# Performance work log

Measured on AMD Instinct MI355X. Metric: run time of the kernel, lower is better.

## Reference

```python
import jax, jax.numpy as jnp
import numpy as np

C = 128
L = 4
NEG_SLOPE = 0.2


def _head(x, rb_w, rb_b, out_w, out_b):
    # x: [T, C]; rb_w: [2, 2, C, C] (block, layer) in torch Linear (out,in) layout.
    for i in range(2):
        h = jax.nn.leaky_relu(x @ rb_w[i, 0].T + rb_b[i, 0], NEG_SLOPE)
        h = h @ rb_w[i, 1].T + rb_b[i, 1]
        x = jax.nn.leaky_relu(x + h, NEG_SLOPE)  # act(shortcut + l2(act(l1(x))))
    return x @ out_w.T + out_b


def setup_inputs() -> dict:
    key = jax.random.key(0)
    ks = iter(jax.random.split(key, 32))
    s = 0.05  # small init so the relu-RNN recurrence stays stable over 32768 steps

    def w(shape):
        return jax.random.normal(next(ks), shape, jnp.float32) * s

    inp = {
        "x": jax.random.normal(next(ks), (C,), jnp.float32),
        "W_ih": w((L, C, C)),
        "W_hh": w((L, C, C)),
        "b_ih": w((L, C)),
        "b_hh": w((L, C)),
    }
    for name, out_dim in [("atom", 8), ("pos", 1), ("mag", 1)]:
        inp[name + "_rb_w"] = w((2, 2, C, C))
        inp[name + "_rb_b"] = w((2, 2, C))
        inp[name + "_w"] = w((out_dim, C))
        inp[name + "_b"] = w((out_dim,))
    inp["max_steps"] = 32768
    return inp


def reference(x, W_ih, W_hh, b_ih, b_hh,
              atom_rb_w, atom_rb_b, atom_w, atom_b,
              pos_rb_w, pos_rb_b, pos_w, pos_b,
              mag_rb_w, mag_rb_b, mag_w, mag_b,
              max_steps):
    # hid[0] = x (conditioning), other layers start at zero; first input is zeros.
    hid0 = jnp.zeros((L, C), x.dtype).at[0].set(x)
    inp0 = jnp.zeros((C,), x.dtype)

    def step(carry, _):
        xin, hid = carry  # xin: [C], hid: [L, C]
        cur = xin
        hs = []
        for l in range(L):
            cur = jax.nn.relu(cur @ W_ih[l].T + b_ih[l] + hid[l] @ W_hh[l].T + b_hh[l])
            hs.append(cur)
        new_hid = jnp.stack(hs)
        return (cur, new_hid), cur  # top-layer output is the next step's input

    _, encodings = jax.lax.scan(step, (inp0, hid0), None, length=max_steps)  # [T, C]

    atoms = _head(encodings, atom_rb_w, atom_rb_b, atom_w, atom_b)  # [T, 8]
    pos = _head(encodings, pos_rb_w, pos_rb_b, pos_w, pos_b)        # [T, 1]
    mags = _head(encodings, mag_rb_w, mag_rb_b, mag_w, mag_b)       # [T, 1]
    return jnp.concatenate([atoms, pos, mags], axis=-1)             # [T, 10]
```

## Files before the change

kernel.cpp:

```cpp
#include <hip/hip_runtime.h>
#include <cstdint>

typedef uint32_t u32;
typedef _Float16 f16;
typedef f16 f16x2 __attribute__((ext_vector_type(2)));
typedef f16 f16x8 __attribute__((ext_vector_type(8)));
typedef float f32x4 __attribute__((ext_vector_type(4)));

static __device__ __forceinline__ u32 pack2(float a, float b) {
    f16x2 v;
    v.x = (f16)a;
    v.y = (f16)b;
    return __builtin_bit_cast(u32, v);
}

static __device__ __forceinline__ float dot2(u32 a, u32 b, float c) {
    return __builtin_amdgcn_fdot2(__builtin_bit_cast(f16x2, a),
                                  __builtin_bit_cast(f16x2, b), c, false);
}

static __device__ __forceinline__ unsigned short f16bits(float v) {
    return __builtin_bit_cast(unsigned short, (f16)v);
}

#define BAR() asm volatile("s_waitcnt lgkmcnt(0)\n\ts_barrier" ::: "memory")

#define MFMA(A, B, C) __builtin_amdgcn_mfma_f32_16x16x32_f16(A, B, C, 0, 0, 0)

__global__ __launch_bounds__(256, 1) void rnn_kernel(
    const float* __restrict__ x0,
    const float* __restrict__ Wih, const float* __restrict__ Whh,
    const float* __restrict__ bih, const float* __restrict__ bhh,
    u32* __restrict__ enc, int T)
{
    __shared__ u32 buf[2][4][64];

    const int tid  = threadIdx.x;
    const int w    = tid >> 6;
    const int lane = tid & 63;
    const int m    = lane & 15;
    const int g    = lane >> 4;

    f16x8 a[4][2][8];
    f32x4 bias[4][2];
    #pragma unroll
    for (int l = 0; l < 4; ++l) {
        #pragma unroll
        for (int t = 0; t < 2; ++t) {
            const int row = w * 32 + t * 16 + m;
            #pragma unroll
            for (int kt = 0; kt < 8; ++kt) {
                const float* W = (kt < 4) ? Wih : Whh;
                const float* p = W + ((size_t)(l * 128 + row)) * 128
                                   + (kt & 3) * 32 + g * 8;
                f16x8 v;
                #pragma unroll
                for (int e = 0; e < 8; ++e) v[e] = (f16)p[e];
                a[l][t][kt] = v;
            }
            const int r4 = w * 32 + t * 16 + g * 4;
            f32x4 b;
            #pragma unroll
            for (int r = 0; r < 4; ++r)
                b[r] = bih[l * 128 + r4 + r] + bhh[l * 128 + r4 + r];
            bias[l][t] = b;
        }
    }

    if (tid < 64)       buf[1][0][tid] = pack2(x0[2 * tid], x0[2 * tid + 1]);
    else if (tid < 256) ((u32*)buf[1])[tid] = 0u;
    __syncthreads();

    f16x8 hpA[4], hpB[4];
    {
        const u32* h0 = &buf[1][0][0];
        #pragma unroll
        for (int j = 0; j < 4; ++j)
            hpA[j] = *(const f16x8*)(h0 + j * 16 + g * 4);
    }

#define SLOT(l, HIN, HOUT, CURB, NXTB, STORE_ENC) do {                        \
        const u32* _cb = (CURB);                                              \
        const u32* _nb = (NXTB);                                              \
        f16x8 i0 = *(const f16x8*)(_cb + 0 * 16 + g * 4);                     \
        f16x8 i1 = *(const f16x8*)(_cb + 1 * 16 + g * 4);                     \
        f16x8 i2 = *(const f16x8*)(_cb + 2 * 16 + g * 4);                     \
        f16x8 i3 = *(const f16x8*)(_cb + 3 * 16 + g * 4);                     \
        HOUT[0] = *(const f16x8*)(_nb + 0 * 16 + g * 4);                      \
        HOUT[1] = *(const f16x8*)(_nb + 1 * 16 + g * 4);                      \
        HOUT[2] = *(const f16x8*)(_nb + 2 * 16 + g * 4);                      \
        HOUT[3] = *(const f16x8*)(_nb + 3 * 16 + g * 4);                      \
        u32* _wb = &buf[_p][l][0];                                            \
        _Pragma("unroll")                                                     \
        for (int t = 0; t < 2; ++t) {                                         \
            f32x4 c0 = bias[l][t];                                            \
            f32x4 c1 = {0.f, 0.f, 0.f, 0.f};                                  \
            c0 = MFMA(a[l][t][4], HIN[0], c0);            \
            c1 = MFMA(a[l][t][5], HIN[1], c1);                                \
            c0 = MFMA(a[l][t][6], HIN[2], c0);                                \
            c1 = MFMA(a[l][t][7], HIN[3], c1);                                \
            c0 = MFMA(a[l][t][0], i0, c0);              \
            c1 = MFMA(a[l][t][1], i1, c1);                                    \
            c0 = MFMA(a[l][t][2], i2, c0);                                    \
            c1 = MFMA(a[l][t][3], i3, c1);                                    \
            f32x4 d = c0 + c1;                                                \
            float y0 = fmaxf(d[0], 0.f), y1 = fmaxf(d[1], 0.f);               \
            float y2 = fmaxf(d[2], 0.f), y3 = fmaxf(d[3], 0.f);               \
            u32 w0 = pack2(y0, y1), w1 = pack2(y2, y3);                       \
            if (m == 0) {                                                     \
                *(uint2*)(_wb + w * 16 + t * 8 + g * 2) = make_uint2(w0, w1); \
                if (STORE_ENC)                                                \
                    *(uint2*)(enc + (size_t)s * 64 + w * 16 + t * 8 + g * 2)  \
                        = make_uint2(w0, w1);                                 \
            }                                                                 \
        }                                                                     \
        BAR();                                                                \
    } while (0)

    for (int s = 0; s < T; ++s) {
        const int _p = s & 1;
        const int _q = _p ^ 1;
        SLOT(0, hpA, hpB, &buf[_q][3][0], &buf[_q][1][0], 0);
        SLOT(1, hpB, hpA, &buf[_p][0][0], &buf[_q][2][0], 0);
        SLOT(2, hpA, hpB, &buf[_p][1][0], &buf[_q][3][0], 0);
        SLOT(3, hpB, hpA, &buf[_p][2][0], &buf[_p][0][0], 1);
    }
#undef SLOT
}

__global__ __launch_bounds__(256) void heads_kernel(
    const u32* __restrict__ enc,
    const float* __restrict__ arw, const float* __restrict__ arb,
    const float* __restrict__ aw,  const float* __restrict__ ab,
    const float* __restrict__ prw, const float* __restrict__ prb,
    const float* __restrict__ pw,  const float* __restrict__ pb,
    const float* __restrict__ mrw, const float* __restrict__ mrb,
    const float* __restrict__ mw,  const float* __restrict__ mb,
    float* __restrict__ out, int T)
{
    const int head = blockIdx.x;
    const int r0 = blockIdx.y * 32;
    if (r0 >= T) return;

    const float *rbw, *rbb, *ow, *ob;
    int od, oc;
    if (head == 0)      { rbw = arw; rbb = arb; ow = aw; ob = ab; od = 8; oc = 0; }
    else if (head == 1) { rbw = prw; rbb = prb; ow = pw; ob = pb; od = 1; oc = 8; }
    else                { rbw = mrw; rbb = mrb; ow = mw; ob = mb; od = 1; oc = 9; }

    __shared__ u32 xs[32][64];
    __shared__ u32 hs[32][64];

    const int tid = threadIdx.x;

    #pragma unroll
    for (int rep = 0; rep < 8; ++rep) {
        int u = tid + rep * 256;
        int row = u >> 6, p = u & 63;
        xs[row][p] = enc[(size_t)(r0 + row) * 64 + p];
    }
    __syncthreads();

    const int j = tid & 127;
    const int rh = tid >> 7;

    float acc[16];
    u32 wreg[64];

#define PACKW(WPTR) do {                                                    \
        const float* _w = (WPTR);                                           \
        _Pragma("unroll")                                                   \
        for (int cc = 0; cc < 16; ++cc) {                                   \
            float4 aa = *(const float4*)(_w + cc * 8);                      \
            float4 bb = *(const float4*)(_w + cc * 8 + 4);                  \
            wreg[cc * 4 + 0] = pack2(aa.x, aa.y);                           \
            wreg[cc * 4 + 1] = pack2(aa.z, aa.w);                           \
            wreg[cc * 4 + 2] = pack2(bb.x, bb.y);                           \
            wreg[cc * 4 + 3] = pack2(bb.z, bb.w);                           \
        }                                                                   \
    } while (0)

#define MM16(SRC) do {                                                      \
        _Pragma("unroll")                                                   \
        for (int r = 0; r < 16; ++r) acc[r] = 0.f;                          \
        _Pragma("unroll")                                                   \
        for (int kp = 0; kp < 16; ++kp) {                                   \
            u32 w0 = wreg[kp * 4 + 0], w1 = wreg[kp * 4 + 1];               \
            u32 w2 = wreg[kp * 4 + 2], w3 = wreg[kp * 4 + 3];               \
            _Pragma("unroll")                                               \
            for (int r = 0; r < 16; ++r) {                                  \
                uint4 x4 = *(const uint4*)(&SRC[rh * 16 + r][kp * 4]);      \
                acc[r] = dot2(x4.x, w0, acc[r]);                            \
                acc[r] = dot2(x4.y, w1, acc[r]);                            \
                acc[r] = dot2(x4.z, w2, acc[r]);                            \
                acc[r] = dot2(x4.w, w3, acc[r]);                            \
            }                                                               \
        }                                                                   \
    } while (0)

    #pragma unroll
    for (int blk = 0; blk < 2; ++blk) {
        PACKW(rbw + (size_t)((blk * 2 + 0) * 128 + j) * 128);
        MM16(xs);
        {
            float b1 = rbb[(blk * 2 + 0) * 128 + j];
            #pragma unroll
            for (int r = 0; r < 16; ++r) {
                float v = acc[r] + b1;
                v = fmaxf(v, 0.2f * v);
                reinterpret_cast<unsigned short*>(&hs[rh * 16 + r][0])[j] = f16bits(v);
            }
        }
        __syncthreads();

        PACKW(rbw + (size_t)((blk * 2 + 1) * 128 + j) * 128);
        MM16(hs);
        {
            float b2 = rbb[(blk * 2 + 1) * 128 + j];
            #pragma unroll
            for (int r = 0; r < 16; ++r) {
                int row = rh * 16 + r;
                unsigned short xb =
                    reinterpret_cast<const unsigned short*>(&xs[row][0])[j];
                float xold = (float)__builtin_bit_cast(f16, xb);
                float v = xold + acc[r] + b2;
                v = fmaxf(v, 0.2f * v);
                reinterpret_cast<unsigned short*>(&xs[row][0])[j] = f16bits(v);
            }
        }
        __syncthreads();
    }

    {
        const int o = tid & 15;
        const int rr = tid >> 4;
        if (o < od) {
            PACKW(ow + (size_t)o * 128);
            float obv = ob[o];
            #pragma unroll
            for (int rs = 0; rs < 2; ++rs) {
                const int row = rr * 2 + rs;
                float a = 0.f;
                #pragma unroll
                for (int kp = 0; kp < 64; ++kp) a = dot2(xs[row][kp], wreg[kp], a);
                out[(size_t)(r0 + row) * 10 + oc + o] = a + obv;
            }
        }
    }
#undef PACKW
#undef MM16
}

extern "C" void kernel_launch(void* const* d_in, const int* in_sizes, int n_in,
                              void* d_out, int out_size, void* d_ws, size_t ws_size,
                              hipStream_t stream)
{
    const float* x   = (const float*)d_in[0];
    const float* Wih = (const float*)d_in[1];
    const float* Whh = (const float*)d_in[2];
    const float* bih = (const float*)d_in[3];
    const float* bhh = (const float*)d_in[4];
    const float* arw = (const float*)d_in[5];
    const float* arb = (const float*)d_in[6];
    const float* aw  = (const float*)d_in[7];
    const float* ab  = (const float*)d_in[8];
    const float* prw = (const float*)d_in[9];
    const float* prb = (const float*)d_in[10];
    const float* pw  = (const float*)d_in[11];
    const float* pb  = (const float*)d_in[12];
    const float* mrw = (const float*)d_in[13];
    const float* mrb = (const float*)d_in[14];
    const float* mw  = (const float*)d_in[15];
    const float* mb  = (const float*)d_in[16];

    const int T = out_size / 10;
    u32* enc = (u32*)d_ws;

    rnn_kernel<<<1, 256, 0, stream>>>(x, Wih, Whh, bih, bhh, enc, T);

    heads_kernel<<<dim3(3, (T + 31) / 32), 256, 0, stream>>>(
        enc, arw, arb, aw, ab, prw, prb, pw, pb, mrw, mrb, mw, mb,
        (float*)d_out, T);
}
```

Before: 39.85 ms.

## Precompute next layer's recurrent term with dot2 off the MFMA critical path

The hidden-to-hidden matvec for the next layer is moved out of the serial per-layer MFMA chain. It is now computed one slot ahead with packed fp16 dot2 instructions on weights held in registers and stored to shared memory as a preactivation. Each slot's critical path then shrinks to four dependent MFMAs on the input term plus the ReLU. In exchange each slot does extra VALU work, holds many more registers (128 u32 of recurrent weights per thread), and adds a shared-memory round trip and a lane shuffle.

```diff
diff --git a/kernel.cpp b/kernel.cpp
--- a/kernel.cpp
+++ b/kernel.cpp
@@ -34,98 +34,142 @@
     u32* __restrict__ enc, int T)
 {
     __shared__ u32 buf[2][4][64];
+    __shared__ float pre[4][128];
 
     const int tid  = threadIdx.x;
     const int w    = tid >> 6;
     const int lane = tid & 63;
     const int m    = lane & 15;
     const int g    = lane >> 4;
-
-    f16x8 a[4][2][8];
-    f32x4 bias[4][2];
+    const int rsh  = w * 32 + (lane >> 1);
+    const int kh   = lane & 1;
+
+    const f32x4 ZERO4 = {0.f, 0.f, 0.f, 0.f};
+
+    f16x8 ihA[4][2][4];
     #pragma unroll
-    for (int l = 0; l < 4; ++l) {
+    for (int l = 0; l < 4; ++l)
         #pragma unroll
         for (int t = 0; t < 2; ++t) {
             const int row = w * 32 + t * 16 + m;
             #pragma unroll
-            for (int kt = 0; kt < 8; ++kt) {
-                const float* W = (kt < 4) ? Wih : Whh;
-                const float* p = W + ((size_t)(l * 128 + row)) * 128
-                                   + (kt & 3) * 32 + g * 8;
+            for (int kt = 0; kt < 4; ++kt) {
+                const float* p = Wih + ((size_t)(l * 128 + row)) * 128
+                                     + kt * 32 + g * 8;
                 f16x8 v;
                 #pragma unroll
                 for (int e = 0; e < 8; ++e) v[e] = (f16)p[e];
-                a[l][t][kt] = v;
+                ihA[l][t][kt] = v;
             }
-            const int r4 = w * 32 + t * 16 + g * 4;
-            f32x4 b;
-            #pragma unroll
-            for (int r = 0; r < 4; ++r)
-                b[r] = bih[l * 128 + r4 + r] + bhh[l * 128 + r4 + r];
-            bias[l][t] = b;
         }
+
+    u32 whd[4][32];
+    float bsh[4];
+    #pragma unroll
+    for (int l = 0; l < 4; ++l) {
+        const float* p = Whh + ((size_t)(l * 128 + rsh)) * 128 + kh * 64;
+        #pragma unroll
+        for (int j = 0; j < 32; ++j)
+            whd[l][j] = pack2(p[2 * j], p[2 * j + 1]);
+        bsh[l] = bih[l * 128 + rsh] + bhh[l * 128 + rsh];
     }
 
     if (tid < 64)       buf[1][0][tid] = pack2(x0[2 * tid], x0[2 * tid + 1]);
     else if (tid < 256) ((u32*)buf[1])[tid] = 0u;
     __syncthreads();
 
-    f16x8 hpA[4], hpB[4];
+#define SHADOW(L, SRC, VOUT) do {                                             \
+        const u32* _hb = &(SRC)[kh * 32];                                     \
+        uint4 h0 = *(const uint4*)(_hb + 0);                                  \
+        uint4 h1 = *(const uint4*)(_hb + 4);                                  \
+        uint4 h2 = *(const uint4*)(_hb + 8);                                  \
+        uint4 h3 = *(const uint4*)(_hb + 12);                                 \
+        uint4 h4 = *(const uint4*)(_hb + 16);                                 \
+        uint4 h5 = *(const uint4*)(_hb + 20);                                 \
+        uint4 h6 = *(const uint4*)(_hb + 24);                                 \
+        uint4 h7 = *(const uint4*)(_hb + 28);                                 \
+        const u32* _wd = whd[L];                                              \
+        float va = kh ? 0.f : bsh[L], vb = 0.f, vc = 0.f, vd = 0.f;           \
+        va = dot2(h0.x, _wd[0], va);  vb = dot2(h0.y, _wd[1], vb);            \
+        vc = dot2(h0.z, _wd[2], vc);  vd = dot2(h0.w, _wd[3], vd);            \
+        va = dot2(h1.x, _wd[4], va);  vb = dot2(h1.y, _wd[5], vb);            \
+        vc = dot2(h1.z, _wd[6], vc);  vd = dot2(h1.w, _wd[7], vd);            \
+        va = dot2(h2.x, _wd[8], va);  vb = dot2(h2.y, _wd[9], vb);            \
+        vc = dot2(h2.z, _wd[10], vc); vd = dot2(h2.w, _wd[11], vd);           \
+        va = dot2(h3.x, _wd[12], va); vb = dot2(h3.y, _wd[13], vb);           \
+        vc = dot2(h3.z, _wd[14], vc); vd = dot2(h3.w, _wd[15], vd);           \
+        va = dot2(h4.x, _wd[16], va); vb = dot2(h4.y, _wd[17], vb);           \
+        vc = dot2(h4.z, _wd[18], vc); vd = dot2(h4.w, _wd[19], vd);           \
+        va = dot2(h5.x, _wd[20], va); vb = dot2(h5.y, _wd[21], vb);           \
+        vc = dot2(h5.z, _wd[22], vc); vd = dot2(h5.w, _wd[23], vd);           \
+        va = dot2(h6.x, _wd[24], va); vb = dot2(h6.y, _wd[25], vb);           \
+        vc = dot2(h6.z, _wd[26], vc); vd = dot2(h6.w, _wd[27], vd);           \
+        va = dot2(h7.x, _wd[28], va); vb = dot2(h7.y, _wd[29], vb);           \
+        vc = dot2(h7.z, _wd[30], vc); vd = dot2(h7.w, _wd[31], vd);           \
+        float _v = (va + vb) + (vc + vd);                                     \
+        _v += __shfl_xor(_v, 1);                                              \
+        VOUT = _v;                                                            \
+    } while (0)
+
     {
-        const u32* h0 = &buf[1][0][0];
-        #pragma unroll
-        for (int j = 0; j < 4; ++j)
-            hpA[j] = *(const f16x8*)(h0 + j * 16 + g * 4);
-    }
-
-#define SLOT(l, HIN, HOUT, CURB, NXTB, STORE_ENC) do {                        \
+        float v;
+        SHADOW(0, buf[1][0], v);
+        if (kh == 0) pre[0][rsh] = v;
+    }
+    __syncthreads();
+
+#define SLOT(l, CURB, SHSRC, STORE_ENC) do {                                  \
+        const int lnx = (l + 1) & 3;                                          \
         const u32* _cb = (CURB);                                              \
-        const u32* _nb = (NXTB);                                              \
+        f32x4 pA = *(const f32x4*)&pre[l][w * 32 + g * 4];                    \
+        f32x4 pB = *(const f32x4*)&pre[l][w * 32 + 16 + g * 4];               \
         f16x8 i0 = *(const f16x8*)(_cb + 0 * 16 + g * 4);                     \
         f16x8 i1 = *(const f16x8*)(_cb + 1 * 16 + g * 4);                     \
         f16x8 i2 = *(const f16x8*)(_cb + 2 * 16 + g * 4);                     \
         f16x8 i3 = *(const f16x8*)(_cb + 3 * 16 + g * 4);                     \
-        HOUT[0] = *(const f16x8*)(_nb + 0 * 16 + g * 4);                      \
-        HOUT[1] = *(const f16x8*)(_nb + 1 * 16 + g * 4);                      \
-        HOUT[2] = *(const f16x8*)(_nb + 2 * 16 + g * 4);                      \
-        HOUT[3] = *(const f16x8*)(_nb + 3 * 16 + g * 4);                      \
+        f32x4 cA0 = MFMA(ihA[l][0][0], i0, pA);                               \
+        f32x4 cB0 = MFMA(ihA[l][0][1], i1, ZERO4);                            \
+        f32x4 cA1 = MFMA(ihA[l][1][0], i0, pB);                               \
+        f32x4 cB1 = MFMA(ihA[l][1][1], i1, ZERO4);                            \
+        cA0 = MFMA(ihA[l][0][2], i2, cA0);                                    \
+        cB0 = MFMA(ihA[l][0][3], i3, cB0);                                    \
+        cA1 = MFMA(ihA[l][1][2], i2, cA1);                                    \
+        cB1 = MFMA(ihA[l][1][3], i3, cB1);                                    \
+        float shv;                                                            \
+        SHADOW(lnx, SHSRC, shv);               \
+        f32x4 d0 = cA0 + cB0;                                                 \
+        f32x4 d1 = cA1 + cB1;                                                 \
         u32* _wb = &buf[_p][l][0];                                            \
-        _Pragma("unroll")                                                     \
-        for (int t = 0; t < 2; ++t) {                                         \
-            f32x4 c0 = bias[l][t];                                            \
-            f32x4 c1 = {0.f, 0.f, 0.f, 0.f};                                  \
-            c0 = MFMA(a[l][t][4], HIN[0], c0);            \
-            c1 = MFMA(a[l][t][5], HIN[1], c1);                                \
-            c0 = MFMA(a[l][t][6], HIN[2], c0);                                \
-            c1 = MFMA(a[l][t][7], HIN[3], c1);                                \
-            c0 = MFMA(a[l][t][0], i0, c0);              \
-            c1 = MFMA(a[l][t][1], i1, c1);                                    \
-            c0 = MFMA(a[l][t][2], i2, c0);                                    \
-            c1 = MFMA(a[l][t][3], i3, c1);                                    \
-            f32x4 d = c0 + c1;                                                \
-            float y0 = fmaxf(d[0], 0.f), y1 = fmaxf(d[1], 0.f);               \
-            float y2 = fmaxf(d[2], 0.f), y3 = fmaxf(d[3], 0.f);               \
-            u32 w0 = pack2(y0, y1), w1 = pack2(y2, y3);                       \
+        {                                                                     \
+            u32 w0 = pack2(fmaxf(d0[0], 0.f), fmaxf(d0[1], 0.f));             \
+            u32 w1 = pack2(fmaxf(d0[2], 0.f), fmaxf(d0[3], 0.f));             \
+            u32 w2 = pack2(fmaxf(d1[0], 0.f), fmaxf(d1[1], 0.f));             \
+            u32 w3 = pack2(fmaxf(d1[2], 0.f), fmaxf(d1[3], 0.f));             \
             if (m == 0) {                                                     \
-                *(uint2*)(_wb + w * 16 + t * 8 + g * 2) = make_uint2(w0, w1); \
-                if (STORE_ENC)                                                \
-                    *(uint2*)(enc + (size_t)s * 64 + w * 16 + t * 8 + g * 2)  \
+                *(uint2*)(_wb + w * 16 + g * 2) = make_uint2(w0, w1);         \
+                *(uint2*)(_wb + w * 16 + 8 + g * 2) = make_uint2(w2, w3);     \
+                if (STORE_ENC) {                                              \
+                    *(uint2*)(enc + (size_t)s * 64 + w * 16 + g * 2)          \
                         = make_uint2(w0, w1);                                 \
+                    *(uint2*)(enc + (size_t)s * 64 + w * 16 + 8 + g * 2)      \
+                        = make_uint2(w2, w3);                                 \
+                }                                                             \
             }                                                                 \
         }                                                                     \
+        if (kh == 0) pre[lnx][rsh] = shv;                                     \
         BAR();                                                                \
     } while (0)
 
     for (int s = 0; s < T; ++s) {
         const int _p = s & 1;
         const int _q = _p ^ 1;
-        SLOT(0, hpA, hpB, &buf[_q][3][0], &buf[_q][1][0], 0);
-        SLOT(1, hpB, hpA, &buf[_p][0][0], &buf[_q][2][0], 0);
-        SLOT(2, hpA, hpB, &buf[_p][1][0], &buf[_q][3][0], 0);
-        SLOT(3, hpB, hpA, &buf[_p][2][0], &buf[_p][0][0], 1);
+        SLOT(0, &buf[_q][3][0], buf[_q][1], 0);
+        SLOT(1, &buf[_p][0][0], buf[_q][2], 0);
+        SLOT(2, &buf[_p][1][0], buf[_q][3], 0);
+        SLOT(3, &buf[_p][2][0], buf[_p][0], 1);
     }
 #undef SLOT
+#undef SHADOW
 }
 
 __global__ __launch_bounds__(256) void heads_kernel(
```

After: 54.50 ms. 1.37x slower.

## Split RNN layer into off-critical-path W_hh MFMA and dot2 W_ih chain

Applied to the files above, without the earlier changes.

Each layer's recurrent W_hh·h term is now computed with MFMA one slot ahead and parked in shared memory, so it runs off the serial dependency chain. The input term W_ih·x on the critical path is done with per-thread packed fp16 dot2 products over half-rows, combined with a lane shuffle, which is meant to cut the latency of each dependent layer step. The step loop is unrolled by two with fixed buffer parities. The cost is more register pressure (W_ih held as 128 packed words per thread) and extra shared-memory traffic for the precomputed sums.

```diff
diff --git a/kernel.cpp b/kernel.cpp
--- a/kernel.cpp
+++ b/kernel.cpp
@@ -34,96 +34,144 @@
     u32* __restrict__ enc, int T)
 {
     __shared__ u32 buf[2][4][64];
+    __shared__ float pre[4][128];
 
     const int tid  = threadIdx.x;
     const int w    = tid >> 6;
     const int lane = tid & 63;
+    const int rsh  = w * 32 + (lane >> 1);
+    const int kh   = lane & 1;
     const int m    = lane & 15;
     const int g    = lane >> 4;
 
-    f16x8 a[4][2][8];
-    f32x4 bias[4][2];
+    u32 wih[4][32];
     #pragma unroll
     for (int l = 0; l < 4; ++l) {
+        const float* p = Wih + ((size_t)(l * 128 + rsh)) * 128 + kh * 64;
+        #pragma unroll
+        for (int j = 0; j < 32; ++j)
+            wih[l][j] = pack2(p[2 * j], p[2 * j + 1]);
+    }
+
+    f16x8 hhA[4][2][4];
+    f32x4 biasT[4][2];
+    #pragma unroll
+    for (int l = 0; l < 4; ++l)
         #pragma unroll
         for (int t = 0; t < 2; ++t) {
             const int row = w * 32 + t * 16 + m;
             #pragma unroll
-            for (int kt = 0; kt < 8; ++kt) {
-                const float* W = (kt < 4) ? Wih : Whh;
-                const float* p = W + ((size_t)(l * 128 + row)) * 128
-                                   + (kt & 3) * 32 + g * 8;
+            for (int kt = 0; kt < 4; ++kt) {
+                const float* p = Whh + ((size_t)(l * 128 + row)) * 128
+                                     + kt * 32 + g * 8;
                 f16x8 v;
                 #pragma unroll
                 for (int e = 0; e < 8; ++e) v[e] = (f16)p[e];
-                a[l][t][kt] = v;
+                hhA[l][t][kt] = v;
             }
             const int r4 = w * 32 + t * 16 + g * 4;
             f32x4 b;
             #pragma unroll
             for (int r = 0; r < 4; ++r)
                 b[r] = bih[l * 128 + r4 + r] + bhh[l * 128 + r4 + r];
-            bias[l][t] = b;
-        }
-    }
+            biasT[l][t] = b;
+        }
 
     if (tid < 64)       buf[1][0][tid] = pack2(x0[2 * tid], x0[2 * tid + 1]);
     else if (tid < 256) ((u32*)buf[1])[tid] = 0u;
     __syncthreads();
 
-    f16x8 hpA[4], hpB[4];
     {
-        const u32* h0 = &buf[1][0][0];
-        #pragma unroll
-        for (int j = 0; j < 4; ++j)
-            hpA[j] = *(const f16x8*)(h0 + j * 16 + g * 4);
-    }
-
-#define SLOT(l, HIN, HOUT, CURB, NXTB, STORE_ENC) do {                        \
-        const u32* _cb = (CURB);                                              \
-        const u32* _nb = (NXTB);                                              \
-        f16x8 i0 = *(const f16x8*)(_cb + 0 * 16 + g * 4);                     \
-        f16x8 i1 = *(const f16x8*)(_cb + 1 * 16 + g * 4);                     \
-        f16x8 i2 = *(const f16x8*)(_cb + 2 * 16 + g * 4);                     \
-        f16x8 i3 = *(const f16x8*)(_cb + 3 * 16 + g * 4);                     \
-        HOUT[0] = *(const f16x8*)(_nb + 0 * 16 + g * 4);                      \
-        HOUT[1] = *(const f16x8*)(_nb + 1 * 16 + g * 4);                      \
-        HOUT[2] = *(const f16x8*)(_nb + 2 * 16 + g * 4);                      \
-        HOUT[3] = *(const f16x8*)(_nb + 3 * 16 + g * 4);                      \
-        u32* _wb = &buf[_p][l][0];                                            \
-        _Pragma("unroll")                                                     \
-        for (int t = 0; t < 2; ++t) {                                         \
-            f32x4 c0 = bias[l][t];                                            \
-            f32x4 c1 = {0.f, 0.f, 0.f, 0.f};                                  \
-            c0 = MFMA(a[l][t][4], HIN[0], c0);            \
-            c1 = MFMA(a[l][t][5], HIN[1], c1);                                \
-            c0 = MFMA(a[l][t][6], HIN[2], c0);                                \
-            c1 = MFMA(a[l][t][7], HIN[3], c1);                                \
-            c0 = MFMA(a[l][t][0], i0, c0);              \
-            c1 = MFMA(a[l][t][1], i1, c1);                                    \
-            c0 = MFMA(a[l][t][2], i2, c0);                                    \
-            c1 = MFMA(a[l][t][3], i3, c1);                                    \
-            f32x4 d = c0 + c1;                                                \
-            float y0 = fmaxf(d[0], 0.f), y1 = fmaxf(d[1], 0.f);               \
-            float y2 = fmaxf(d[2], 0.f), y3 = fmaxf(d[3], 0.f);               \
-            u32 w0 = pack2(y0, y1), w1 = pack2(y2, y3);                       \
-            if (m == 0) {                                                     \
-                *(uint2*)(_wb + w * 16 + t * 8 + g * 2) = make_uint2(w0, w1); \
-                if (STORE_ENC)                                                \
-                    *(uint2*)(enc + (size_t)s * 64 + w * 16 + t * 8 + g * 2)  \
-                        = make_uint2(w0, w1);                                 \
-            }                                                                 \
+        const u32* sb = &buf[1][0][0];
+        f16x8 j0 = *(const f16x8*)(sb + 0 * 16 + g * 4);
+        f16x8 j1 = *(const f16x8*)(sb + 1 * 16 + g * 4);
+        f16x8 j2 = *(const f16x8*)(sb + 2 * 16 + g * 4);
+        f16x8 j3 = *(const f16x8*)(sb + 3 * 16 + g * 4);
+        f32x4 t0 = MFMA(hhA[0][0][0], j0, biasT[0][0]);
+        t0 = MFMA(hhA[0][0][1], j1, t0);
+        t0 = MFMA(hhA[0][0][2], j2, t0);
+        t0 = MFMA(hhA[0][0][3], j3, t0);
+        f32x4 t1 = MFMA(hhA[0][1][0], j0, biasT[0][1]);
+        t1 = MFMA(hhA[0][1][1], j1, t1);
+        t1 = MFMA(hhA[0][1][2], j2, t1);
+        t1 = MFMA(hhA[0][1][3], j3, t1);
+        if (m == 0) {
+            *(f32x4*)&pre[0][w * 32 + g * 4] = t0;
+            *(f32x4*)&pre[0][w * 32 + 16 + g * 4] = t1;
+        }
+    }
+    f32x4 pa0, pa1;
+    f32x4 pb0 = biasT[1][0], pb1 = biasT[1][1];
+    BAR();
+
+#define SLOT(l, P, CURB, SHB, LT, LW, PI0, PI1, PW0, PW1, STORE, S) do {      \
+        float pr = pre[l][rsh];                                               \
+        const u32* _yb = (CURB) + kh * 32;                                    \
+        uint4 h0 = *(const uint4*)(_yb + 0);                                  \
+        uint4 h1 = *(const uint4*)(_yb + 4);                                  \
+        uint4 h2 = *(const uint4*)(_yb + 8);                                  \
+        uint4 h3 = *(const uint4*)(_yb + 12);                                 \
+        uint4 h4 = *(const uint4*)(_yb + 16);                                 \
+        uint4 h5 = *(const uint4*)(_yb + 20);                                 \
+        uint4 h6 = *(const uint4*)(_yb + 24);                                 \
+        uint4 h7 = *(const uint4*)(_yb + 28);                                 \
+        const u32* _wd = wih[l];                                              \
+        float va = kh ? 0.f : pr, vb = 0.f, vc = 0.f, vd = 0.f;               \
+        va = dot2(h0.x, _wd[0], va);  vb = dot2(h0.y, _wd[1], vb);            \
+        vc = dot2(h0.z, _wd[2], vc);  vd = dot2(h0.w, _wd[3], vd);            \
+        va = dot2(h1.x, _wd[4], va);  vb = dot2(h1.y, _wd[5], vb);            \
+        vc = dot2(h1.z, _wd[6], vc);  vd = dot2(h1.w, _wd[7], vd);            \
+        va = dot2(h2.x, _wd[8], va);  vb = dot2(h2.y, _wd[9], vb);            \
+        vc = dot2(h2.z, _wd[10], vc); vd = dot2(h2.w, _wd[11], vd);           \
+        va = dot2(h3.x, _wd[12], va); vb = dot2(h3.y, _wd[13], vb);           \
+        vc = dot2(h3.z, _wd[14], vc); vd = dot2(h3.w, _wd[15], vd);           \
+        va = dot2(h4.x, _wd[16], va); vb = dot2(h4.y, _wd[17], vb);           \
+        vc = dot2(h4.z, _wd[18], vc); vd = dot2(h4.w, _wd[19], vd);           \
+        va = dot2(h5.x, _wd[20], va); vb = dot2(h5.y, _wd[21], vb);           \
+        vc = dot2(h5.z, _wd[22], vc); vd = dot2(h5.w, _wd[23], vd);           \
+        va = dot2(h6.x, _wd[24], va); vb = dot2(h6.y, _wd[25], vb);           \
+        vc = dot2(h6.z, _wd[26], vc); vd = dot2(h6.w, _wd[27], vd);           \
+        va = dot2(h7.x, _wd[28], va); vb = dot2(h7.y, _wd[29], vb);           \
+        vc = dot2(h7.z, _wd[30], vc); vd = dot2(h7.w, _wd[31], vd);           \
+        float v = (va + vb) + (vc + vd);                                      \
+        v += __shfl_xor(v, 1);                                                \
+        float y = fmaxf(v, 0.f);                                              \
+        float yo = __shfl_xor(y, 2);                                          \
+        if ((lane & 3) == 0) {                                                \
+            u32 pk = pack2(y, yo);                                            \
+            buf[P][l][w * 16 + (lane >> 2)] = pk;                             \
+            if (STORE)                                                        \
+                enc[(size_t)(S) * 64 + w * 16 + (lane >> 2)] = pk;            \
         }                                                                     \
+        if (m == 0) {                                                         \
+            *(f32x4*)&pre[LW][w * 32 + g * 4] = PW0;                          \
+            *(f32x4*)&pre[LW][w * 32 + 16 + g * 4] = PW1;                     \
+        }                                                                     \
+        const u32* _sb = (SHB);                                               \
+        f16x8 j0 = *(const f16x8*)(_sb + 0 * 16 + g * 4);                     \
+        f16x8 j1 = *(const f16x8*)(_sb + 1 * 16 + g * 4);                     \
+        f16x8 j2 = *(const f16x8*)(_sb + 2 * 16 + g * 4);                     \
+        f16x8 j3 = *(const f16x8*)(_sb + 3 * 16 + g * 4);                     \
+        PI0 = MFMA(hhA[LT][0][0], j0, biasT[LT][0]);                          \
+        PI0 = MFMA(hhA[LT][0][1], j1, PI0);                                   \
+        PI0 = MFMA(hhA[LT][0][2], j2, PI0);                                   \
+        PI0 = MFMA(hhA[LT][0][3], j3, PI0);                                   \
+        PI1 = MFMA(hhA[LT][1][0], j0, biasT[LT][1]);                          \
+        PI1 = MFMA(hhA[LT][1][1], j1, PI1);                                   \
+        PI1 = MFMA(hhA[LT][1][2], j2, PI1);                                   \
+        PI1 = MFMA(hhA[LT][1][3], j3, PI1);                                   \
         BAR();                                                                \
     } while (0)
 
-    for (int s = 0; s < T; ++s) {
-        const int _p = s & 1;
-        const int _q = _p ^ 1;
-        SLOT(0, hpA, hpB, &buf[_q][3][0], &buf[_q][1][0], 0);
-        SLOT(1, hpB, hpA, &buf[_p][0][0], &buf[_q][2][0], 0);
-        SLOT(2, hpA, hpB, &buf[_p][1][0], &buf[_q][3][0], 0);
-        SLOT(3, hpB, hpA, &buf[_p][2][0], &buf[_p][0][0], 1);
+    for (int s = 0; s < T; s += 2) {
+        SLOT(0, 0, &buf[1][3][0], &buf[1][2][0], 2, 1, pa0, pa1, pb0, pb1, 0, s);
+        SLOT(1, 0, &buf[0][0][0], &buf[1][3][0], 3, 2, pb0, pb1, pa0, pa1, 0, s);
+        SLOT(2, 0, &buf[0][1][0], &buf[0][0][0], 0, 3, pa0, pa1, pb0, pb1, 0, s);
+        SLOT(3, 0, &buf[0][2][0], &buf[0][1][0], 1, 0, pb0, pb1, pa0, pa1, 1, s);
+        SLOT(0, 1, &buf[0][3][0], &buf[0][2][0], 2, 1, pa0, pa1, pb0, pb1, 0, s + 1);
+        SLOT(1, 1, &buf[1][0][0], &buf[0][3][0], 3, 2, pb0, pb1, pa0, pa1, 0, s + 1);
+        SLOT(2, 1, &buf[1][1][0], &buf[1][0][0], 0, 3, pa0, pa1, pb0, pb1, 0, s + 1);
+        SLOT(3, 1, &buf[1][2][0], &buf[1][1][0], 1, 0, pb0, pb1, pa0, pa1, 1, s + 1);
     }
 #undef SLOT
 }
```

Result: slower. 53.76 ms (+34.9%).
